# Optimization experiments

Measured on AMD Instinct MI355X. Metric: run time of the kernel, lower is better.

The kernel has to match this reference:

```python
import jax, jax.numpy as jnp
import numpy as np

D, Z, A, H, E = 1024, 256, 32, 512, 1024  # deterministic, state, action, stochastic(hidden), embedding
MIN_STD = 0.1


def _linear_params(key, out_dim, in_dim, scale=0.02):
    kw, kb = jax.random.split(key)
    W = jax.random.normal(kw, (out_dim, in_dim), jnp.float32) * scale
    b = jax.random.normal(kb, (out_dim,), jnp.float32) * scale
    return W, b


def setup_inputs() -> dict:
    key = jax.random.key(0)
    ks = jax.random.split(key, 16)
    T, B = 64, 512
    inp = {
        "prev_state": jax.random.normal(ks[0], (B, Z), jnp.float32),
        "prev_belief": jax.random.normal(ks[1], (B, D), jnp.float32),
        "actions": jax.random.normal(ks[2], (T, B, A), jnp.float32),
        "observations": jax.random.normal(ks[3], (T, B, E), jnp.float32),
        "nonterminals": jnp.ones((T, B, 1), jnp.float32),
        "noise_belief": jax.random.normal(ks[4], (T, B, D), jnp.float32),
        "noise_prior": jax.random.normal(ks[5], (T, B, Z), jnp.float32),
        "noise_post": jax.random.normal(ks[6], (T, B, Z), jnp.float32),
    }
    inp["W_sa"], inp["b_sa"] = _linear_params(ks[7], D, Z + A)      # fc_embed_state_action
    inp["W_ih"], inp["b_ih"] = _linear_params(ks[8], 3 * D, D)       # GRUCell input weights
    inp["W_hh"], inp["b_hh"] = _linear_params(ks[9], 3 * D, D)       # GRUCell hidden weights
    inp["W_eb"], inp["b_eb"] = _linear_params(ks[10], H, D)          # fc_embed_belief
    inp["W_bq"], inp["b_bq"] = _linear_params(ks[11], 2 * D, H)      # fc_belief_posterior
    inp["W_ebp"], inp["b_ebp"] = _linear_params(ks[12], H, D)        # fc_embed_belief_prior
    inp["W_sp"], inp["b_sp"] = _linear_params(ks[13], 2 * Z, H)      # fc_state_prior
    inp["W_ebq"], inp["b_ebq"] = _linear_params(ks[14], H, D + E)    # fc_embed_belief_posterior
    inp["W_sq"], inp["b_sq"] = _linear_params(ks[15], 2 * Z, H)      # fc_state_posterior
    return inp


def _gru_cell(x, h, W_ih, b_ih, W_hh, b_hh):
    gi = x @ W_ih.T + b_ih
    gh = h @ W_hh.T + b_hh
    i_r, i_z, i_n = jnp.split(gi, 3, axis=-1)
    h_r, h_z, h_n = jnp.split(gh, 3, axis=-1)
    r = jax.nn.sigmoid(i_r + h_r)
    z = jax.nn.sigmoid(i_z + h_z)
    n = jnp.tanh(i_n + r * h_n)
    return (1.0 - z) * n + z * h


def rssm_scan(prev_state, prev_belief, actions, observations, nonterminals,
              noise_belief, noise_prior, noise_post,
              W_sa, b_sa, W_ih, b_ih, W_hh, b_hh, W_eb, b_eb, W_bq, b_bq,
              W_ebp, b_ebp, W_sp, b_sp, W_ebq, b_ebq, W_sq, b_sq):
    # t==0 skips the nonterminal mask; shift nonterminals by one and prepend ones
    nt_seq = jnp.concatenate([jnp.ones_like(nonterminals[:1]), nonterminals[:-1]], axis=0)

    def step(carry, xs):
        belief, state = carry
        a_t, o_t, nt_t, nb_t, np_t, nq_t = xs
        s = state * nt_t
        deter_hidden = jax.nn.relu(jnp.concatenate([s, a_t], axis=1) @ W_sa.T + b_sa)
        rnn_out = _gru_cell(deter_hidden, belief, W_ih, b_ih, W_hh, b_hh)
        # stochastic belief
        sh = jax.nn.relu(rnn_out @ W_eb.T + b_eb)
        b_mean, b_raw_std = jnp.split(sh @ W_bq.T + b_bq, 2, axis=1)
        b_std = jax.nn.softplus(b_raw_std) + MIN_STD
        new_belief = b_mean + b_std * nb_t
        # prior
        sh_p = jax.nn.relu(new_belief @ W_ebp.T + b_ebp)
        p_mean, p_raw_std = jnp.split(sh_p @ W_sp.T + b_sp, 2, axis=1)
        p_std = jax.nn.softplus(p_raw_std) + MIN_STD
        p_state = p_mean + p_std * np_t
        # posterior (observations provided)
        sh_q = jax.nn.relu(jnp.concatenate([new_belief, o_t], axis=1) @ W_ebq.T + b_ebq)
        q_mean, q_raw_std = jnp.split(sh_q @ W_sq.T + b_sq, 2, axis=1)
        q_std = jax.nn.softplus(q_raw_std) + MIN_STD
        q_state = q_mean + q_std * nq_t
        return (new_belief, q_state), (new_belief, p_state, p_mean, p_std, q_state, q_mean, q_std)

    xs = (actions, observations, nt_seq, noise_belief, noise_prior, noise_post)
    _, ys = jax.lax.scan(step, (prev_belief, prev_state), xs)
    return ys  # each [T, B, dim]


def reference(prev_state, prev_belief, actions, observations, nonterminals,
              noise_belief, noise_prior, noise_post,
              W_sa, b_sa, W_ih, b_ih, W_hh, b_hh, W_eb, b_eb, W_bq, b_bq,
              W_ebp, b_ebp, W_sp, b_sp, W_ebq, b_ebq, W_sq, b_sq):
    return rssm_scan(prev_state, prev_belief, actions, observations, nonterminals,
                     noise_belief, noise_prior, noise_post,
                     W_sa, b_sa, W_ih, b_ih, W_hh, b_hh, W_eb, b_eb, W_bq, b_bq,
                     W_ebp, b_ebp, W_sp, b_sp, W_ebq, b_ebq, W_sq, b_sq)
```

## Files before the change

### kernel.cpp

```cpp
#include <hip/hip_runtime.h>
#include <hip/hip_bf16.h>
#include <math.h>


using bf16 = __hip_bfloat16;
using short8 = __attribute__((ext_vector_type(8))) short;
using f32x4 = __attribute__((ext_vector_type(4))) float;

__device__ __forceinline__ float sp_f(float x) { return x > 15.f ? x : log1pf(__expf(x)); }
__device__ __forceinline__ float sg_f(float x) { return 1.f / (1.f + __expf(-x)); }

struct GArgs {
  const bf16* Ab;
  const float* Af;
  const bf16* Bw;
  const float* bias;
  float* Cf;
  bf16* Cb;
  const float* addmat;
  const float* s_src;
  const float* nt_src;
  const float* act_src;
  int M, N, K, ldb, ldc, ldadd;
};

template<int ASRC, int EPI>
__device__ void gemm_core(const GArgs g, int bid) {
  __shared__ bf16 As[128 * 32];
  __shared__ bf16 Bs[128 * 32];
  const int ntiles = g.N >> 7;
  const int mt = bid / ntiles, nt = bid % ntiles;
  const int tid = threadIdx.x;
  const int l = tid & 63, w = tid >> 6;
  const int wm = w >> 1, wn = w & 1;
  const int l4r = l >> 2, l4b = l & 3;
  const int fl = l & 15, fg = l >> 4;
  f32x4 acc[4][4] = {};

  for (int k0 = 0; k0 < g.K; k0 += 32) {
    if constexpr (ASRC == 0) {
#pragma unroll
      for (int i = 0; i < 2; ++i) {
        const int r = w * 32 + i * 16;
        const bf16* gp = g.Ab + (size_t)(mt * 128 + r + l4r) * g.K + k0 + l4b * 8;
        __builtin_amdgcn_global_load_lds((const __attribute__((address_space(1))) void*)gp,
                                         (__attribute__((address_space(3))) void*)(As + r * 32),
                                         16, 0, 0);
      }
    } else {
#pragma unroll
      for (int p = 0; p < 2; ++p) {
        const int e = p * 2048 + tid * 8;
        const int r = e >> 5, c = e & 31;
        const int rg = mt * 128 + r;
        float4 x0, x1;
        if constexpr (ASRC == 1) {
          const float* src = g.Af + (size_t)rg * g.K + k0 + c;
          x0 = *(const float4*)src; x1 = *(const float4*)(src + 4);
        } else {
          const int kg = k0 + c;
          if (kg < 256) {
            const float* src = g.s_src + rg * 256 + kg;
            x0 = *(const float4*)src; x1 = *(const float4*)(src + 4);
            const float ntv = g.nt_src ? g.nt_src[rg] : 1.f;
            x0.x *= ntv; x0.y *= ntv; x0.z *= ntv; x0.w *= ntv;
            x1.x *= ntv; x1.y *= ntv; x1.z *= ntv; x1.w *= ntv;
          } else {
            const float* src = g.act_src + rg * 32 + (kg - 256);
            x0 = *(const float4*)src; x1 = *(const float4*)(src + 4);
          }
        }
        bf16 tb[8] __attribute__((aligned(16)));
        tb[0] = __float2bfloat16(x0.x); tb[1] = __float2bfloat16(x0.y);
        tb[2] = __float2bfloat16(x0.z); tb[3] = __float2bfloat16(x0.w);
        tb[4] = __float2bfloat16(x1.x); tb[5] = __float2bfloat16(x1.y);
        tb[6] = __float2bfloat16(x1.z); tb[7] = __float2bfloat16(x1.w);
        *(short8*)(As + e) = *(const short8*)tb;
      }
    }
#pragma unroll
    for (int i = 0; i < 2; ++i) {
      const int r = w * 32 + i * 16;
      const bf16* gp = g.Bw + (size_t)(nt * 128 + r + l4r) * g.ldb + k0 + l4b * 8;
      __builtin_amdgcn_global_load_lds((const __attribute__((address_space(1))) void*)gp,
                                       (__attribute__((address_space(3))) void*)(Bs + r * 32),
                                       16, 0, 0);
    }
    __syncthreads();
    short8 afr[4], bfr[4];
#pragma unroll
    for (int i = 0; i < 4; ++i)
      afr[i] = *(const short8*)(As + (wm * 64 + i * 16 + fl) * 32 + fg * 8);
#pragma unroll
    for (int i = 0; i < 4; ++i)
      bfr[i] = *(const short8*)(Bs + (wn * 64 + i * 16 + fl) * 32 + fg * 8);
#pragma unroll
    for (int mf = 0; mf < 4; ++mf)
#pragma unroll
      for (int nf = 0; nf < 4; ++nf)
        asm("v_mfma_f32_16x16x32_bf16 %0, %1, %2, %0"
            : "+v"(acc[mf][nf]) : "v"(afr[mf]), "v"(bfr[nf]));
    __syncthreads();
  }
#pragma unroll
  for (int mf = 0; mf < 4; ++mf) {
#pragma unroll
    for (int nf = 0; nf < 4; ++nf) {
      const int col = nt * 128 + wn * 64 + nf * 16 + fl;
      const float bv = g.bias ? g.bias[col] : 0.f;
#pragma unroll
      for (int r = 0; r < 4; ++r) {
        const int row = mt * 128 + wm * 64 + mf * 16 + fg * 4 + r;
        float v = acc[mf][nf][r] + bv;
        if constexpr (EPI == 2) v += g.addmat[(size_t)row * g.ldadd + col];
        if constexpr (EPI == 0) {
          g.Cf[(size_t)row * g.ldc + col] = v;
        } else {
          v = v > 0.f ? v : 0.f;
          g.Cb[(size_t)row * g.ldc + col] = __float2bfloat16(v);
        }
      }
    }
  }
}

template<int ASRC, int EPI>
__global__ __launch_bounds__(256) void gemm_k(GArgs g) { gemm_core<ASRC, EPI>(g, blockIdx.x); }

__global__ __launch_bounds__(256) void gemm2_k(GArgs g0, GArgs g1, int nb0) {
  if ((int)blockIdx.x < nb0) gemm_core<0, 0>(g0, blockIdx.x);
  else                       gemm_core<0, 0>(g1, blockIdx.x - nb0);
}

__global__ __launch_bounds__(256) void cvt_k(const float* __restrict__ src, bf16* __restrict__ dst, int n4) {
  int i = blockIdx.x * 256 + threadIdx.x;
  if (i >= n4) return;
  float4 v = ((const float4*)src)[i];
  bf16 t[4] __attribute__((aligned(8)));
  t[0] = __float2bfloat16(v.x); t[1] = __float2bfloat16(v.y);
  t[2] = __float2bfloat16(v.z); t[3] = __float2bfloat16(v.w);
  ((uint2*)dst)[i] = *(const uint2*)t;
}

__global__ __launch_bounds__(256) void gates_k(const float* __restrict__ gi, const float* __restrict__ gh,
                                               const bf16* __restrict__ hprev, bf16* __restrict__ rnn) {
  int i = blockIdx.x * 256 + threadIdx.x;
  if (i >= 512 * 1024) return;
  int m = i >> 10, n = i & 1023;
  const float* gim = gi + (size_t)m * 3072;
  const float* ghm = gh + (size_t)m * 3072;
  float r = sg_f(gim[n] + ghm[n]);
  float z = sg_f(gim[1024 + n] + ghm[1024 + n]);
  float nn = tanhf(gim[2048 + n] + r * ghm[2048 + n]);
  float h = __bfloat162float(hprev[i]);
  rnn[i] = __float2bfloat16((1.f - z) * nn + z * h);
}

__global__ __launch_bounds__(256) void belief_k(const float* __restrict__ raw, const float* __restrict__ nb,
                                                float* __restrict__ obel, bf16* __restrict__ bbf) {
  int i = blockIdx.x * 256 + threadIdx.x;
  if (i >= 512 * 1024) return;
  int m = i >> 10, n = i & 1023;
  float mean = raw[(size_t)m * 2048 + n];
  float rs = raw[(size_t)m * 2048 + 1024 + n];
  float sd = sp_f(rs) + 0.1f;
  float b = mean + sd * nb[i];
  obel[i] = b;
  bbf[i] = __float2bfloat16(b);
}

__global__ __launch_bounds__(256) void qpost_k(const float* __restrict__ raw, const float* __restrict__ noise,
                                               float* __restrict__ om, float* __restrict__ os,
                                               float* __restrict__ ost, int n) {
  int i = blockIdx.x * 256 + threadIdx.x;
  if (i >= n) return;
  int m = i >> 8, z = i & 255;
  float mean = raw[(size_t)m * 512 + z];
  float rs = raw[(size_t)m * 512 + 256 + z];
  float sd = sp_f(rs) + 0.1f;
  om[i] = mean; os[i] = sd; ost[i] = mean + sd * noise[i];
}

extern "C" void kernel_launch(void* const* d_in, const int* in_sizes, int n_in,
                              void* d_out, int out_size, void* d_ws, size_t ws_size,
                              hipStream_t stream) {
  const float* prev_state   = (const float*)d_in[0];
  const float* prev_belief  = (const float*)d_in[1];
  const float* actions      = (const float*)d_in[2];
  const float* observations = (const float*)d_in[3];
  const float* nonterm      = (const float*)d_in[4];
  const float* noise_belief = (const float*)d_in[5];
  const float* noise_prior  = (const float*)d_in[6];
  const float* noise_post   = (const float*)d_in[7];
  const float* W_sa  = (const float*)d_in[8];  const float* b_sa  = (const float*)d_in[9];
  const float* W_ih  = (const float*)d_in[10]; const float* b_ih  = (const float*)d_in[11];
  const float* W_hh  = (const float*)d_in[12]; const float* b_hh  = (const float*)d_in[13];
  const float* W_eb  = (const float*)d_in[14]; const float* b_eb  = (const float*)d_in[15];
  const float* W_bq  = (const float*)d_in[16]; const float* b_bq  = (const float*)d_in[17];
  const float* W_ebp = (const float*)d_in[18]; const float* b_ebp = (const float*)d_in[19];
  const float* W_sp  = (const float*)d_in[20]; const float* b_sp  = (const float*)d_in[21];
  const float* W_ebq = (const float*)d_in[22]; const float* b_ebq = (const float*)d_in[23];
  const float* W_sq  = (const float*)d_in[24]; const float* b_sq  = (const float*)d_in[25];

  float* out = (float*)d_out;
  const size_t off_bel = 0;
  const size_t off_pst = 33554432;
  const size_t off_pm  = 41943040;
  const size_t off_psd = 50331648;
  const size_t off_qst = 58720256;
  const size_t off_qm  = 67108864;
  const size_t off_qsd = 75497472;

  char* ws = (char*)d_ws;
  bf16* wbf   = (bf16*)ws;
  bf16* w_sa  = wbf;
  bf16* w_ih  = wbf + 294912;
  bf16* w_hh  = wbf + 3440640;
  bf16* w_eb  = wbf + 6586368;
  bf16* w_bq  = wbf + 7110656;
  bf16* w_ebp = wbf + 8159232;
  bf16* w_sp  = wbf + 8683520;
  bf16* w_ebq = wbf + 8945664;
  bf16* w_sq  = wbf + 9994240;
  size_t p = 20971520;
  bf16* bel_bf   = (bf16*)(ws + p); p += 1048576;
  bf16* deter_bf = (bf16*)(ws + p); p += 1048576;
  bf16* rnn_bf   = (bf16*)(ws + p); p += 1048576;
  bf16* sh_bf    = (bf16*)(ws + p); p += 524288;
  bf16* shq_bf   = (bf16*)(ws + p); p += 524288;
  float* p_raw = (float*)(ws + 25165824);
  float *gi, *gh, *bq_raw, *q_raw;
  if (ws_size >= 42991616ull) {
    gi     = (float*)(ws + 25165824);
    gh     = (float*)(ws + 31457280);
    bq_raw = (float*)(ws + 37748736);
    q_raw  = (float*)(ws + 41943040);
  } else {
    float* scratch = out + off_pst;
    gi = scratch; gh = scratch + 1572864; bq_raw = gh + 1572864; q_raw = bq_raw + 1048576;
  }

  auto cvt = [&](const float* s, bf16* d, int n) {
    int n4 = n >> 2;
    cvt_k<<<(n4 + 255) / 256, 256, 0, stream>>>(s, d, n4);
  };
  cvt(W_sa, w_sa, 294912);   cvt(W_ih, w_ih, 3145728);  cvt(W_hh, w_hh, 3145728);
  cvt(W_eb, w_eb, 524288);   cvt(W_bq, w_bq, 1048576);  cvt(W_ebp, w_ebp, 524288);
  cvt(W_sp, w_sp, 262144);   cvt(W_ebq, w_ebq, 1048576); cvt(W_sq, w_sq, 262144);
  cvt(prev_belief, bel_bf, 524288);

  float* obs_c = out + off_pm;
  {
    GArgs g{}; g.Af = observations; g.Bw = w_ebq + 1024; g.ldb = 2048; g.bias = b_ebq;
    g.Cf = obs_c; g.ldc = 512; g.M = 32768; g.N = 512; g.K = 1024;
    gemm_k<1, 0><<<1024, 256, 0, stream>>>(g);
  }

  for (int t = 0; t < 64; ++t) {
    {
      GArgs g{};
      g.s_src  = (t == 0) ? prev_state : out + off_qst + (size_t)(t - 1) * 131072;
      g.nt_src = (t == 0) ? nullptr : nonterm + (size_t)(t - 1) * 512;
      g.act_src = actions + (size_t)t * 16384;
      g.Bw = w_sa; g.ldb = 288; g.bias = b_sa; g.Cb = deter_bf; g.ldc = 1024;
      g.M = 512; g.N = 1024; g.K = 288;
      gemm_k<2, 1><<<32, 256, 0, stream>>>(g);
    }
    {
      GArgs g0{}; g0.Ab = deter_bf; g0.Bw = w_ih; g0.ldb = 1024; g0.bias = b_ih;
      g0.Cf = gi; g0.ldc = 3072; g0.M = 512; g0.N = 3072; g0.K = 1024;
      GArgs g1 = g0; g1.Ab = bel_bf; g1.Bw = w_hh; g1.bias = b_hh; g1.Cf = gh;
      gemm2_k<<<192, 256, 0, stream>>>(g0, g1, 96);
    }
    gates_k<<<2048, 256, 0, stream>>>(gi, gh, bel_bf, rnn_bf);
    {
      GArgs g{}; g.Ab = rnn_bf; g.Bw = w_eb; g.ldb = 1024; g.bias = b_eb;
      g.Cb = sh_bf; g.ldc = 512; g.M = 512; g.N = 512; g.K = 1024;
      gemm_k<0, 1><<<16, 256, 0, stream>>>(g);
    }
    {
      GArgs g{}; g.Ab = sh_bf; g.Bw = w_bq; g.ldb = 512; g.bias = b_bq;
      g.Cf = bq_raw; g.ldc = 2048; g.M = 512; g.N = 2048; g.K = 512;
      gemm_k<0, 0><<<64, 256, 0, stream>>>(g);
    }
    belief_k<<<2048, 256, 0, stream>>>(bq_raw, noise_belief + (size_t)t * 524288,
                                       out + off_bel + (size_t)t * 524288, bel_bf);
    {
      GArgs g{}; g.Ab = bel_bf; g.Bw = w_ebq; g.ldb = 2048;
      g.addmat = obs_c + (size_t)t * 262144; g.ldadd = 512;
      g.Cb = shq_bf; g.ldc = 512; g.M = 512; g.N = 512; g.K = 1024;
      gemm_k<0, 2><<<16, 256, 0, stream>>>(g);
    }
    {
      GArgs g{}; g.Ab = shq_bf; g.Bw = w_sq; g.ldb = 512; g.bias = b_sq;
      g.Cf = q_raw; g.ldc = 512; g.M = 512; g.N = 512; g.K = 512;
      gemm_k<0, 0><<<16, 256, 0, stream>>>(g);
    }
    qpost_k<<<512, 256, 0, stream>>>(q_raw, noise_post + (size_t)t * 131072,
                                     out + off_qm + (size_t)t * 131072,
                                     out + off_qsd + (size_t)t * 131072,
                                     out + off_qst + (size_t)t * 131072, 131072);
  }

  bf16* shp = (bf16*)(out + off_pst);
  {
    GArgs g{}; g.Af = out + off_bel; g.Bw = w_ebp; g.ldb = 1024; g.bias = b_ebp;
    g.Cb = shp; g.ldc = 512; g.M = 32768; g.N = 512; g.K = 1024;
    gemm_k<1, 1><<<1024, 256, 0, stream>>>(g);
  }
  for (int c = 0; c < 16; ++c) {
    {
      GArgs g{}; g.Ab = shp + (size_t)c * 1048576; g.Bw = w_sp; g.ldb = 512; g.bias = b_sp;
      g.Cf = p_raw; g.ldc = 512; g.M = 2048; g.N = 512; g.K = 512;
      gemm_k<0, 0><<<64, 256, 0, stream>>>(g);
    }
    qpost_k<<<2048, 256, 0, stream>>>(p_raw, noise_prior + (size_t)c * 524288,
                                      out + off_pm + (size_t)c * 524288,
                                      out + off_psd + (size_t)c * 524288,
                                      out + off_pst + (size_t)c * 524288, 524288);
  }
}
```

Measured before the change: 10.07 ms.

## Replace per-step kernel launches with persistent kernel using grid barriers and fused epilogues

Replaces the many per-timestep GEMM and elementwise launches with one persistent kernel of 128 blocks that synchronises stages through a hand-written global atomic barrier. The GRU input and hidden GEMMs are merged by interleaving reordered weights, so the gate math, belief sampling and posterior sampling run in GEMM epilogues instead of in separate kernels over fp32 scratch. LDS tiles grow to K=64 with an XOR swizzle and double-buffered async loads. This targets launch overhead and intermediate memory traffic in the sequential scan. It risks deadlock if all 128 blocks are not co-resident, and adds barrier latency at every stage.

```diff
diff --git a/kernel.cpp b/kernel.cpp
--- a/kernel.cpp
+++ b/kernel.cpp
@@ -7,178 +7,455 @@
 using short8 = __attribute__((ext_vector_type(8))) short;
 using f32x4 = __attribute__((ext_vector_type(4))) float;
 
-__device__ __forceinline__ float sp_f(float x) { return x > 15.f ? x : log1pf(__expf(x)); }
-__device__ __forceinline__ float sg_f(float x) { return 1.f / (1.f + __expf(-x)); }
-
-struct GArgs {
-  const bf16* Ab;
-  const float* Af;
-  const bf16* Bw;
-  const float* bias;
-  float* Cf;
-  bf16* Cb;
-  const float* addmat;
-  const float* s_src;
-  const float* nt_src;
-  const float* act_src;
-  int M, N, K, ldb, ldc, ldadd;
-};
-
-template<int ASRC, int EPI>
-__device__ void gemm_core(const GArgs g, int bid) {
-  __shared__ bf16 As[128 * 32];
-  __shared__ bf16 Bs[128 * 32];
-  const int ntiles = g.N >> 7;
-  const int mt = bid / ntiles, nt = bid % ntiles;
-  const int tid = threadIdx.x;
-  const int l = tid & 63, w = tid >> 6;
-  const int wm = w >> 1, wn = w & 1;
-  const int l4r = l >> 2, l4b = l & 3;
-  const int fl = l & 15, fg = l >> 4;
-  f32x4 acc[4][4] = {};
-
-  for (int k0 = 0; k0 < g.K; k0 += 32) {
-    if constexpr (ASRC == 0) {
-#pragma unroll
-      for (int i = 0; i < 2; ++i) {
-        const int r = w * 32 + i * 16;
-        const bf16* gp = g.Ab + (size_t)(mt * 128 + r + l4r) * g.K + k0 + l4b * 8;
-        __builtin_amdgcn_global_load_lds((const __attribute__((address_space(1))) void*)gp,
-                                         (__attribute__((address_space(3))) void*)(As + r * 32),
-                                         16, 0, 0);
-      }
-    } else {
-#pragma unroll
-      for (int p = 0; p < 2; ++p) {
-        const int e = p * 2048 + tid * 8;
-        const int r = e >> 5, c = e & 31;
-        const int rg = mt * 128 + r;
-        float4 x0, x1;
-        if constexpr (ASRC == 1) {
-          const float* src = g.Af + (size_t)rg * g.K + k0 + c;
-          x0 = *(const float4*)src; x1 = *(const float4*)(src + 4);
-        } else {
-          const int kg = k0 + c;
-          if (kg < 256) {
-            const float* src = g.s_src + rg * 256 + kg;
-            x0 = *(const float4*)src; x1 = *(const float4*)(src + 4);
-            const float ntv = g.nt_src ? g.nt_src[rg] : 1.f;
-            x0.x *= ntv; x0.y *= ntv; x0.z *= ntv; x0.w *= ntv;
-            x1.x *= ntv; x1.y *= ntv; x1.z *= ntv; x1.w *= ntv;
-          } else {
-            const float* src = g.act_src + rg * 32 + (kg - 256);
-            x0 = *(const float4*)src; x1 = *(const float4*)(src + 4);
-          }
-        }
-        bf16 tb[8] __attribute__((aligned(16)));
-        tb[0] = __float2bfloat16(x0.x); tb[1] = __float2bfloat16(x0.y);
-        tb[2] = __float2bfloat16(x0.z); tb[3] = __float2bfloat16(x0.w);
-        tb[4] = __float2bfloat16(x1.x); tb[5] = __float2bfloat16(x1.y);
-        tb[6] = __float2bfloat16(x1.z); tb[7] = __float2bfloat16(x1.w);
-        *(short8*)(As + e) = *(const short8*)tb;
-      }
-    }
-#pragma unroll
-    for (int i = 0; i < 2; ++i) {
-      const int r = w * 32 + i * 16;
-      const bf16* gp = g.Bw + (size_t)(nt * 128 + r + l4r) * g.ldb + k0 + l4b * 8;
-      __builtin_amdgcn_global_load_lds((const __attribute__((address_space(1))) void*)gp,
-                                       (__attribute__((address_space(3))) void*)(Bs + r * 32),
-                                       16, 0, 0);
+#define GRID 128
+
+__device__ __forceinline__ float sp_f(float x){ return x > 15.f ? x : log1pf(__expf(x)); }
+__device__ __forceinline__ float sg_f(float x){ return 1.f/(1.f+__expf(-x)); }
+__device__ __forceinline__ float b2f(bf16 x){ return __bfloat162float(x); }
+__device__ __forceinline__ bf16  f2b(float x){ return __float2bfloat16(x); }
+
+__device__ __forceinline__ int lds_off(int row, int slot){ return row*64 + (((slot ^ (row & 7))) << 3); }
+
+__device__ __forceinline__ void gbar(int* arrive, int* go, int ev) {
+  __threadfence();
+  __syncthreads();
+  if (blockIdx.x == 0) {
+    const int t = threadIdx.x;
+    if (t > 0 && t < GRID) {
+      while (__hip_atomic_load(&arrive[t], __ATOMIC_ACQUIRE, __HIP_MEMORY_SCOPE_AGENT) < ev)
+        __builtin_amdgcn_s_sleep(1);
     }
     __syncthreads();
-    short8 afr[4], bfr[4];
+    if (t == 0) __hip_atomic_store(go, ev, __ATOMIC_RELEASE, __HIP_MEMORY_SCOPE_AGENT);
+  } else {
+    if (threadIdx.x == 0) {
+      __hip_atomic_store(&arrive[blockIdx.x], ev, __ATOMIC_RELEASE, __HIP_MEMORY_SCOPE_AGENT);
+      while (__hip_atomic_load(go, __ATOMIC_ACQUIRE, __HIP_MEMORY_SCOPE_AGENT) < ev)
+        __builtin_amdgcn_s_sleep(1);
+    }
+  }
+  __syncthreads();
+  __threadfence();
+}
+
+__device__ __forceinline__ void glds_tile(const bf16* base, int ld, bf16* buf, int w, int l) {
+  const int rsub = l >> 3;
+  const int slot = (l & 7) ^ rsub;
+  const bf16* src = base + (size_t)(w*32 + rsub)*ld + slot*8;
+#pragma unroll
+  for (int i = 0; i < 4; ++i)
+    __builtin_amdgcn_global_load_lds((const __attribute__((address_space(1))) void*)(src + (size_t)(i*8)*ld),
+                                     (__attribute__((address_space(3))) void*)(buf + (w*32 + i*8)*64),
+                                     16, 0, 0);
+}
+
+__device__ __forceinline__ void mfma_tiles(f32x4 acc[4][4], const bf16* bA, const bf16* bB,
+                                           int wm, int wn, int fl, int fg) {
+#pragma unroll
+  for (int ks = 0; ks < 2; ++ks) {
+    short8 af[4], bfr[4];
 #pragma unroll
     for (int i = 0; i < 4; ++i)
-      afr[i] = *(const short8*)(As + (wm * 64 + i * 16 + fl) * 32 + fg * 8);
+      af[i] = *(const short8*)(bA + lds_off(wm*64 + i*16 + fl, ks*4 + fg));
 #pragma unroll
     for (int i = 0; i < 4; ++i)
-      bfr[i] = *(const short8*)(Bs + (wn * 64 + i * 16 + fl) * 32 + fg * 8);
+      bfr[i] = *(const short8*)(bB + lds_off(wn*64 + i*16 + fl, ks*4 + fg));
 #pragma unroll
     for (int mf = 0; mf < 4; ++mf)
 #pragma unroll
       for (int nf = 0; nf < 4; ++nf)
         asm("v_mfma_f32_16x16x32_bf16 %0, %1, %2, %0"
-            : "+v"(acc[mf][nf]) : "v"(afr[mf]), "v"(bfr[nf]));
-    __syncthreads();
-  }
-#pragma unroll
-  for (int mf = 0; mf < 4; ++mf) {
+            : "+v"(acc[mf][nf]) : "v"(af[mf]), "v"(bfr[nf]));
+  }
+}
+
+template<bool GRUA>
+__device__ __forceinline__ void kloop_async(const bf16* A0, const bf16* A1, int lda,
+    const bf16* Bw, int ldb, int K, int mt, int nt, f32x4 acc[4][4],
+    int w, int l, int wm, int wn, int fl, int fg,
+    bf16* sA0, bf16* sA1, bf16* sB0, bf16* sB1) {
+  bf16* bufA[2] = {sA0, sA1};
+  bf16* bufB[2] = {sB0, sB1};
+  const int nk = K >> 6;
+  glds_tile(A0 + (size_t)(mt*128)*lda, lda, bufA[0], w, l);
+  glds_tile(Bw + (size_t)(nt*128)*ldb, ldb, bufB[0], w, l);
+#pragma unroll 1
+  for (int ki = 0; ki < nk; ++ki) {
+    const int kn = ki + 1;
+    if (kn < nk) {
+      const int k0 = kn << 6;
+      const bf16* As; int kc;
+      if (GRUA && k0 >= 1024) { As = A1; kc = k0 - 1024; } else { As = A0; kc = k0; }
+      glds_tile(As + (size_t)(mt*128)*lda + kc, lda, bufA[kn & 1], w, l);
+      glds_tile(Bw + (size_t)(nt*128)*ldb + k0, ldb, bufB[kn & 1], w, l);
+      asm volatile("s_waitcnt vmcnt(8)" ::: "memory");
+    } else {
+      asm volatile("s_waitcnt vmcnt(0)" ::: "memory");
+    }
+    __builtin_amdgcn_s_barrier();
+    asm volatile("" ::: "memory");
+    mfma_tiles(acc, bufA[ki & 1], bufB[ki & 1], wm, wn, fl, fg);
+    asm volatile("" ::: "memory");
+    __builtin_amdgcn_s_barrier();
+    asm volatile("" ::: "memory");
+  }
+}
+
+__device__ __forceinline__ void kloop_sync_f32(const float* A, int lda, const bf16* Bw, int ldb,
+    int K, int mt, int nt, f32x4 acc[4][4],
+    int tid, int w, int l, int wm, int wn, int fl, int fg, bf16* sA0, bf16* sB0) {
+  const int nk = K >> 6;
+#pragma unroll 1
+  for (int ki = 0; ki < nk; ++ki) {
+    const int k0 = ki << 6;
+    glds_tile(Bw + (size_t)(nt*128)*ldb + k0, ldb, sB0, w, l);
+#pragma unroll
+    for (int i = 0; i < 4; ++i) {
+      const int sid = tid + (i << 8);
+      const int row = sid >> 3, s = sid & 7;
+      const float* src = A + (size_t)(mt*128 + row)*lda + k0 + s*8;
+      float4 a = ((const float4*)src)[0], b = ((const float4*)src)[1];
+      bf16 t8[8] __attribute__((aligned(16)));
+      t8[0]=f2b(a.x); t8[1]=f2b(a.y); t8[2]=f2b(a.z); t8[3]=f2b(a.w);
+      t8[4]=f2b(b.x); t8[5]=f2b(b.y); t8[6]=f2b(b.z); t8[7]=f2b(b.w);
+      *(short8*)(sA0 + lds_off(row, s)) = *(const short8*)t8;
+    }
+    asm volatile("s_waitcnt vmcnt(0) lgkmcnt(0)" ::: "memory");
+    __builtin_amdgcn_s_barrier();
+    asm volatile("" ::: "memory");
+    mfma_tiles(acc, sA0, sB0, wm, wn, fl, fg);
+    asm volatile("" ::: "memory");
+    __builtin_amdgcn_s_barrier();
+    asm volatile("" ::: "memory");
+  }
+}
+
+__device__ __forceinline__ void kloop_sa(const float* st, const float* ntp, const float* act,
+    const bf16* Bw, int mt, int nt, f32x4 acc[4][4],
+    int tid, int w, int l, int wm, int wn, int fl, int fg, bf16* sA0, bf16* sB0) {
+#pragma unroll 1
+  for (int ki = 0; ki < 5; ++ki) {
+    const int k0 = ki << 6;
+    glds_tile(Bw + (size_t)(nt*128)*320 + k0, 320, sB0, w, l);
+#pragma unroll
+    for (int i = 0; i < 4; ++i) {
+      const int sid = tid + (i << 8);
+      const int row = sid >> 3, s = sid & 7;
+      const int rg = mt*128 + row;
+      const int kg = k0 + s*8;
+      float4 a = {0,0,0,0}, b = {0,0,0,0};
+      if (kg < 256) {
+        const float* src = st + (size_t)rg*256 + kg;
+        a = ((const float4*)src)[0]; b = ((const float4*)src)[1];
+        const float nv = ntp ? ntp[rg] : 1.f;
+        a.x*=nv; a.y*=nv; a.z*=nv; a.w*=nv; b.x*=nv; b.y*=nv; b.z*=nv; b.w*=nv;
+      } else if (kg < 288) {
+        const float* src = act + (size_t)rg*32 + (kg - 256);
+        a = ((const float4*)src)[0]; b = ((const float4*)src)[1];
+      }
+      bf16 t8[8] __attribute__((aligned(16)));
+      t8[0]=f2b(a.x); t8[1]=f2b(a.y); t8[2]=f2b(a.z); t8[3]=f2b(a.w);
+      t8[4]=f2b(b.x); t8[5]=f2b(b.y); t8[6]=f2b(b.z); t8[7]=f2b(b.w);
+      *(short8*)(sA0 + lds_off(row, s)) = *(const short8*)t8;
+    }
+    asm volatile("s_waitcnt vmcnt(0) lgkmcnt(0)" ::: "memory");
+    __builtin_amdgcn_s_barrier();
+    asm volatile("" ::: "memory");
+    mfma_tiles(acc, sA0, sB0, wm, wn, fl, fg);
+    asm volatile("" ::: "memory");
+    __builtin_amdgcn_s_barrier();
+    asm volatile("" ::: "memory");
+  }
+}
+
+template<bool RELU, bool ADD>
+__device__ __forceinline__ void epi_bf16(const f32x4 acc[4][4], bf16* dst, int ldc,
+    const float* bias, const bf16* addm, int lda2, int mt, int nt, int wm, int wn, int fl, int fg) {
+#pragma unroll
+  for (int mf = 0; mf < 4; ++mf)
 #pragma unroll
     for (int nf = 0; nf < 4; ++nf) {
-      const int col = nt * 128 + wn * 64 + nf * 16 + fl;
-      const float bv = g.bias ? g.bias[col] : 0.f;
+      const int col = nt*128 + wn*64 + nf*16 + fl;
+      const float bv = bias ? bias[col] : 0.f;
 #pragma unroll
       for (int r = 0; r < 4; ++r) {
-        const int row = mt * 128 + wm * 64 + mf * 16 + fg * 4 + r;
+        const int row = mt*128 + wm*64 + mf*16 + fg*4 + r;
         float v = acc[mf][nf][r] + bv;
-        if constexpr (EPI == 2) v += g.addmat[(size_t)row * g.ldadd + col];
-        if constexpr (EPI == 0) {
-          g.Cf[(size_t)row * g.ldc + col] = v;
-        } else {
-          v = v > 0.f ? v : 0.f;
-          g.Cb[(size_t)row * g.ldc + col] = __float2bfloat16(v);
-        }
+        if (ADD) v += b2f(addm[(size_t)row*lda2 + col]);
+        if (RELU) v = v > 0.f ? v : 0.f;
+        dst[(size_t)row*ldc + col] = f2b(v);
       }
     }
-  }
-}
-
-template<int ASRC, int EPI>
-__global__ __launch_bounds__(256) void gemm_k(GArgs g) { gemm_core<ASRC, EPI>(g, blockIdx.x); }
-
-__global__ __launch_bounds__(256) void gemm2_k(GArgs g0, GArgs g1, int nb0) {
-  if ((int)blockIdx.x < nb0) gemm_core<0, 0>(g0, blockIdx.x);
-  else                       gemm_core<0, 0>(g1, blockIdx.x - nb0);
-}
-
-__global__ __launch_bounds__(256) void cvt_k(const float* __restrict__ src, bf16* __restrict__ dst, int n4) {
-  int i = blockIdx.x * 256 + threadIdx.x;
-  if (i >= n4) return;
-  float4 v = ((const float4*)src)[i];
-  bf16 t[4] __attribute__((aligned(8)));
-  t[0] = __float2bfloat16(v.x); t[1] = __float2bfloat16(v.y);
-  t[2] = __float2bfloat16(v.z); t[3] = __float2bfloat16(v.w);
-  ((uint2*)dst)[i] = *(const uint2*)t;
-}
-
-__global__ __launch_bounds__(256) void gates_k(const float* __restrict__ gi, const float* __restrict__ gh,
-                                               const bf16* __restrict__ hprev, bf16* __restrict__ rnn) {
-  int i = blockIdx.x * 256 + threadIdx.x;
-  if (i >= 512 * 1024) return;
-  int m = i >> 10, n = i & 1023;
-  const float* gim = gi + (size_t)m * 3072;
-  const float* ghm = gh + (size_t)m * 3072;
-  float r = sg_f(gim[n] + ghm[n]);
-  float z = sg_f(gim[1024 + n] + ghm[1024 + n]);
-  float nn = tanhf(gim[2048 + n] + r * ghm[2048 + n]);
-  float h = __bfloat162float(hprev[i]);
-  rnn[i] = __float2bfloat16((1.f - z) * nn + z * h);
-}
-
-__global__ __launch_bounds__(256) void belief_k(const float* __restrict__ raw, const float* __restrict__ nb,
-                                                float* __restrict__ obel, bf16* __restrict__ bbf) {
-  int i = blockIdx.x * 256 + threadIdx.x;
-  if (i >= 512 * 1024) return;
-  int m = i >> 10, n = i & 1023;
-  float mean = raw[(size_t)m * 2048 + n];
-  float rs = raw[(size_t)m * 2048 + 1024 + n];
-  float sd = sp_f(rs) + 0.1f;
-  float b = mean + sd * nb[i];
-  obel[i] = b;
-  bbf[i] = __float2bfloat16(b);
-}
-
-__global__ __launch_bounds__(256) void qpost_k(const float* __restrict__ raw, const float* __restrict__ noise,
-                                               float* __restrict__ om, float* __restrict__ os,
-                                               float* __restrict__ ost, int n) {
-  int i = blockIdx.x * 256 + threadIdx.x;
-  if (i >= n) return;
-  int m = i >> 8, z = i & 255;
-  float mean = raw[(size_t)m * 512 + z];
-  float rs = raw[(size_t)m * 512 + 256 + z];
-  float sd = sp_f(rs) + 0.1f;
-  om[i] = mean; os[i] = sd; ost[i] = mean + sd * noise[i];
+}
+
+__device__ __forceinline__ void epi_gru(const f32x4 acc[4][4], const float* bg,
+    const bf16* bel, bf16* rnn, int mt, int nt, int wm, int wn, int fl, int fg) {
+  const int cb = nt*128 + wn*64;
+  const int j = nt*32 + wn*16 + fl;
+  const float b0 = bg[cb + fl], b1 = bg[cb + 16 + fl], b2 = bg[cb + 32 + fl], b3 = bg[cb + 48 + fl];
+#pragma unroll
+  for (int mf = 0; mf < 4; ++mf)
+#pragma unroll
+    for (int r = 0; r < 4; ++r) {
+      const int row = mt*128 + wm*64 + mf*16 + fg*4 + r;
+      const float a0 = acc[mf][0][r] + b0;
+      const float a1 = acc[mf][1][r] + b1;
+      const float a2 = acc[mf][2][r] + b2;
+      const float a3 = acc[mf][3][r] + b3;
+      const float rr = sg_f(a0), zz = sg_f(a1);
+      const float nn = tanhf(a2 + rr*a3);
+      const float h = b2f(bel[(size_t)row*1024 + j]);
+      rnn[(size_t)row*1024 + j] = f2b((1.f - zz)*nn + zz*h);
+    }
+}
+
+__device__ __forceinline__ void epi_bq(const f32x4 acc[4][4], const float* bb,
+    const float* nb, float* obel, bf16* belbf, int mt, int nt, int wm, int wn, int fl, int fg) {
+  const int cb = nt*128 + wn*64;
+#pragma unroll
+  for (int g = 0; g < 2; ++g) {
+    const int j = nt*64 + (wn*2 + g)*16 + fl;
+    const float bm = bb[cb + g*32 + fl];
+    const float bs = bb[cb + g*32 + 16 + fl];
+#pragma unroll
+    for (int mf = 0; mf < 4; ++mf)
+#pragma unroll
+      for (int r = 0; r < 4; ++r) {
+        const int row = mt*128 + wm*64 + mf*16 + fg*4 + r;
+        const float mean = acc[mf][2*g][r] + bm;
+        const float sd = sp_f(acc[mf][2*g+1][r] + bs) + 0.1f;
+        const float bl = mean + sd * nb[(size_t)row*1024 + j];
+        obel[(size_t)row*1024 + j] = bl;
+        belbf[(size_t)row*1024 + j] = f2b(bl);
+      }
+  }
+}
+
+__device__ __forceinline__ void epi_qp(const f32x4 acc[4][4], const float* bb, const float* noise,
+    float* om, float* os, float* ost, int mt, int nt, int wm, int wn, int fl, int fg) {
+  const int cb = nt*128 + wn*64;
+#pragma unroll
+  for (int g = 0; g < 2; ++g) {
+    const int j = nt*64 + (wn*2 + g)*16 + fl;
+    const float bm = bb[cb + g*32 + fl];
+    const float bs = bb[cb + g*32 + 16 + fl];
+#pragma unroll
+    for (int mf = 0; mf < 4; ++mf)
+#pragma unroll
+      for (int r = 0; r < 4; ++r) {
+        const int row = mt*128 + wm*64 + mf*16 + fg*4 + r;
+        const float mean = acc[mf][2*g][r] + bm;
+        const float sd = sp_f(acc[mf][2*g+1][r] + bs) + 0.1f;
+        const size_t o = (size_t)row*256 + j;
+        om[o] = mean; os[o] = sd; ost[o] = mean + sd*noise[o];
+      }
+  }
+}
+
+struct PP {
+  const float *prev_state, *prev_belief, *actions, *obs, *nonterm, *nb, *np, *nq;
+  const float *b_sa, *b_eb, *b_ebq, *b_ebp;
+  const bf16 *w_sa, *w_gru, *w_eb, *w_bq, *w_ebq, *w_sq, *w_ebp, *w_sp;
+  const float *bg, *bbq, *bsq, *bsp;
+  bf16 *obs_c, *deter, *bel, *rnn, *sh, *shq, *shp;
+  float *o_bel, *o_pst, *o_pm, *o_psd, *o_qst, *o_qm, *o_qsd;
+  int *arrive; int *go;
+};
+
+__global__ __launch_bounds__(256) void persist_k(PP p) {
+  __shared__ bf16 sA[2][8192];
+  __shared__ bf16 sB[2][8192];
+  const int bid = blockIdx.x, tid = threadIdx.x;
+  const int l = tid & 63, w = tid >> 6;
+  const int wm = w >> 1, wn = w & 1, fl = l & 15, fg = l >> 4;
+  int ev = 1;
+
+#pragma unroll 1
+  for (int i = bid*256 + tid; i < 65536; i += GRID*256) {
+    float4 a = ((const float4*)p.prev_belief)[i*2];
+    float4 b = ((const float4*)p.prev_belief)[i*2 + 1];
+    bf16 t8[8] __attribute__((aligned(16)));
+    t8[0]=f2b(a.x); t8[1]=f2b(a.y); t8[2]=f2b(a.z); t8[3]=f2b(a.w);
+    t8[4]=f2b(b.x); t8[5]=f2b(b.y); t8[6]=f2b(b.z); t8[7]=f2b(b.w);
+    ((short8*)p.bel)[i] = *(const short8*)t8;
+  }
+#pragma unroll 1
+  for (int tt = bid; tt < 1024; tt += GRID) {
+    const int mt = tt >> 2, nt = tt & 3;
+    f32x4 acc[4][4] = {};
+    kloop_sync_f32(p.obs, 1024, p.w_ebq + 1024, 2048, 1024, mt, nt, acc,
+                   tid, w, l, wm, wn, fl, fg, sA[0], sB[0]);
+    epi_bf16<false,false>(acc, p.obs_c, 512, p.b_ebq, nullptr, 0, mt, nt, wm, wn, fl, fg);
+  }
+  gbar(p.arrive, p.go, ev++);
+
+#pragma unroll 1
+  for (int t = 0; t < 64; ++t) {
+    if (bid < 32) {
+      const int mt = bid >> 3, nt = bid & 7;
+      f32x4 acc[4][4] = {};
+      const float* ss  = t ? (p.o_qst + (size_t)(t-1)*131072) : p.prev_state;
+      const float* ntp = t ? (p.nonterm + (size_t)(t-1)*512) : nullptr;
+      kloop_sa(ss, ntp, p.actions + (size_t)t*16384, p.w_sa, mt, nt, acc,
+               tid, w, l, wm, wn, fl, fg, sA[0], sB[0]);
+      epi_bf16<true,false>(acc, p.deter, 1024, p.b_sa, nullptr, 0, mt, nt, wm, wn, fl, fg);
+    }
+    gbar(p.arrive, p.go, ev++);
+    {
+      const int mt = bid >> 5, nt = bid & 31;
+      f32x4 acc[4][4] = {};
+      kloop_async<true>(p.deter, p.bel, 1024, p.w_gru, 2048, 2048, mt, nt, acc,
+                        w, l, wm, wn, fl, fg, sA[0], sA[1], sB[0], sB[1]);
+      epi_gru(acc, p.bg, p.bel, p.rnn, mt, nt, wm, wn, fl, fg);
+    }
+    gbar(p.arrive, p.go, ev++);
+    if (bid < 16) {
+      const int mt = bid >> 2, nt = bid & 3;
+      f32x4 acc[4][4] = {};
+      kloop_async<false>(p.rnn, nullptr, 1024, p.w_eb, 1024, 1024, mt, nt, acc,
+                         w, l, wm, wn, fl, fg, sA[0], sA[1], sB[0], sB[1]);
+      epi_bf16<true,false>(acc, p.sh, 512, p.b_eb, nullptr, 0, mt, nt, wm, wn, fl, fg);
+    }
+    gbar(p.arrive, p.go, ev++);
+    if (bid < 64) {
+      const int mt = bid >> 4, nt = bid & 15;
+      f32x4 acc[4][4] = {};
+      kloop_async<false>(p.sh, nullptr, 512, p.w_bq, 512, 512, mt, nt, acc,
+                         w, l, wm, wn, fl, fg, sA[0], sA[1], sB[0], sB[1]);
+      epi_bq(acc, p.bbq, p.nb + (size_t)t*524288, p.o_bel + (size_t)t*524288, p.bel,
+             mt, nt, wm, wn, fl, fg);
+    }
+    gbar(p.arrive, p.go, ev++);
+    if (bid < 16) {
+      const int mt = bid >> 2, nt = bid & 3;
+      f32x4 acc[4][4] = {};
+      kloop_async<false>(p.bel, nullptr, 1024, p.w_ebq, 2048, 1024, mt, nt, acc,
+                         w, l, wm, wn, fl, fg, sA[0], sA[1], sB[0], sB[1]);
+      epi_bf16<true,true>(acc, p.shq, 512, nullptr, p.obs_c + (size_t)t*262144, 512,
+                          mt, nt, wm, wn, fl, fg);
+    }
+    gbar(p.arrive, p.go, ev++);
+    if (bid < 16) {
+      const int mt = bid >> 2, nt = bid & 3;
+      f32x4 acc[4][4] = {};
+      kloop_async<false>(p.shq, nullptr, 512, p.w_sq, 512, 512, mt, nt, acc,
+                         w, l, wm, wn, fl, fg, sA[0], sA[1], sB[0], sB[1]);
+      epi_qp(acc, p.bsq, p.nq + (size_t)t*131072,
+             p.o_qm + (size_t)t*131072, p.o_qsd + (size_t)t*131072, p.o_qst + (size_t)t*131072,
+             mt, nt, wm, wn, fl, fg);
+    }
+    gbar(p.arrive, p.go, ev++);
+  }
+
+#pragma unroll 1
+  for (int tt = bid; tt < 1024; tt += GRID) {
+    const int mt = tt >> 2, nt = tt & 3;
+    f32x4 acc[4][4] = {};
+    kloop_sync_f32(p.o_bel, 1024, p.w_ebp, 1024, 1024, mt, nt, acc,
+                   tid, w, l, wm, wn, fl, fg, sA[0], sB[0]);
+    epi_bf16<true,false>(acc, p.shp, 512, p.b_ebp, nullptr, 0, mt, nt, wm, wn, fl, fg);
+  }
+  gbar(p.arrive, p.go, ev++);
+#pragma unroll 1
+  for (int c = 0; c < 8; ++c) {
+    const int mt = c*32 + (bid >> 2), nt = bid & 3;
+    f32x4 acc[4][4] = {};
+    kloop_async<false>(p.shp, nullptr, 512, p.w_sp, 512, 512, mt, nt, acc,
+                       w, l, wm, wn, fl, fg, sA[0], sA[1], sB[0], sB[1]);
+    gbar(p.arrive, p.go, ev++);
+    epi_qp(acc, p.bsp, p.np, p.o_pm, p.o_psd, p.o_pst, mt, nt, wm, wn, fl, fg);
+  }
+}
+
+__global__ __launch_bounds__(256) void k_cvt8(const float* __restrict__ s, bf16* __restrict__ d, int n8) {
+  int i = blockIdx.x*256 + threadIdx.x;
+  if (i >= n8) return;
+  float4 a = ((const float4*)s)[i*2], b = ((const float4*)s)[i*2+1];
+  bf16 t8[8] __attribute__((aligned(16)));
+  t8[0]=f2b(a.x); t8[1]=f2b(a.y); t8[2]=f2b(a.z); t8[3]=f2b(a.w);
+  t8[4]=f2b(b.x); t8[5]=f2b(b.y); t8[6]=f2b(b.z); t8[7]=f2b(b.w);
+  ((short8*)d)[i] = *(const short8*)t8;
+}
+
+__global__ __launch_bounds__(256) void k_wsa(const float* __restrict__ W, bf16* __restrict__ dst) {
+  int i = blockIdx.x*256 + threadIdx.x;
+  if (i >= 40960) return;
+  int e = i*8, r = e/320, c = e - r*320;
+  bf16 t8[8] __attribute__((aligned(16)));
+  if (c < 288) {
+    const float* s = W + (size_t)r*288 + c;
+    float4 a = ((const float4*)s)[0], b = ((const float4*)s)[1];
+    t8[0]=f2b(a.x); t8[1]=f2b(a.y); t8[2]=f2b(a.z); t8[3]=f2b(a.w);
+    t8[4]=f2b(b.x); t8[5]=f2b(b.y); t8[6]=f2b(b.z); t8[7]=f2b(b.w);
+  } else {
+    for (int q = 0; q < 8; ++q) t8[q] = f2b(0.f);
+  }
+  *(short8*)(dst + e) = *(const short8*)t8;
+}
+
+__global__ __launch_bounds__(256) void k_gru_r(const float* __restrict__ Wih, const float* __restrict__ Whh,
+                                               bf16* __restrict__ dst) {
+  int idx = blockIdx.x*256 + threadIdx.x;
+  if (idx >= 2097152) return;
+  int rp = idx >> 9;
+  int c4 = (idx & 511) << 2;
+  int nt = rp >> 7, id = rp & 127;
+  int wn2 = (id >> 6) & 1, nf = (id >> 4) & 3, fl2 = id & 15;
+  int j = nt*32 + wn2*16 + fl2;
+  float4 v = {0,0,0,0};
+  if (c4 < 1024) {
+    int srow = (nf==0) ? j : (nf==1) ? 1024+j : (nf==2) ? 2048+j : -1;
+    if (srow >= 0) v = *(const float4*)(Wih + (size_t)srow*1024 + c4);
+  } else {
+    int srow = (nf==0) ? j : (nf==1) ? 1024+j : (nf==3) ? 2048+j : -1;
+    if (srow >= 0) v = *(const float4*)(Whh + (size_t)srow*1024 + (c4-1024));
+  }
+  bf16 t4[4] __attribute__((aligned(8)));
+  t4[0]=f2b(v.x); t4[1]=f2b(v.y); t4[2]=f2b(v.z); t4[3]=f2b(v.w);
+  *(uint2*)(dst + (size_t)rp*2048 + c4) = *(const uint2*)t4;
+}
+
+__global__ __launch_bounds__(256) void k_pair(const float* __restrict__ src, bf16* __restrict__ dst,
+                                              int halfN, int n) {
+  int idx = blockIdx.x*256 + threadIdx.x;
+  if (idx >= n) return;
+  int rp = idx >> 7;
+  int c4 = (idx & 127) << 2;
+  int nt = rp >> 7, id = rp & 127;
+  int pb = (id >> 5) & 3, comp = (id >> 4) & 1, fl2 = id & 15;
+  int j = nt*64 + pb*16 + fl2;
+  int srow = comp*halfN + j;
+  float4 v = *(const float4*)(src + (size_t)srow*512 + c4);
+  bf16 t4[4] __attribute__((aligned(8)));
+  t4[0]=f2b(v.x); t4[1]=f2b(v.y); t4[2]=f2b(v.z); t4[3]=f2b(v.w);
+  *(uint2*)(dst + (size_t)rp*512 + c4) = *(const uint2*)t4;
+}
+
+__global__ __launch_bounds__(256) void k_bias(const float* b_ih, const float* b_hh, const float* b_bq,
+                                              const float* b_sq, const float* b_sp,
+                                              float* bg, float* bbq, float* bsq, float* bsp) {
+  for (int i = threadIdx.x; i < 4096; i += 256) {
+    int nt = i >> 7, id = i & 127;
+    int wn2 = (id >> 6) & 1, nf = (id >> 4) & 3, fl2 = id & 15;
+    int j = nt*32 + wn2*16 + fl2;
+    float v;
+    if (nf == 0) v = b_ih[j] + b_hh[j];
+    else if (nf == 1) v = b_ih[1024+j] + b_hh[1024+j];
+    else if (nf == 2) v = b_ih[2048+j];
+    else v = b_hh[2048+j];
+    bg[i] = v;
+  }
+  for (int i = threadIdx.x; i < 2048; i += 256) {
+    int nt = i >> 7, id = i & 127, pb = (id >> 5) & 3, comp = (id >> 4) & 1, fl2 = id & 15;
+    int j = nt*64 + pb*16 + fl2;
+    bbq[i] = b_bq[comp*1024 + j];
+  }
+  for (int i = threadIdx.x; i < 512; i += 256) {
+    int nt = i >> 7, id = i & 127, pb = (id >> 5) & 3, comp = (id >> 4) & 1, fl2 = id & 15;
+    int j = nt*64 + pb*16 + fl2;
+    bsq[i] = b_sq[comp*256 + j];
+    bsp[i] = b_sp[comp*256 + j];
+  }
 }
 
 extern "C" void kernel_launch(void* const* d_in, const int* in_sizes, int n_in,
@@ -203,120 +480,61 @@
   const float* W_sq  = (const float*)d_in[24]; const float* b_sq  = (const float*)d_in[25];
 
   float* out = (float*)d_out;
-  const size_t off_bel = 0;
-  const size_t off_pst = 33554432;
-  const size_t off_pm  = 41943040;
-  const size_t off_psd = 50331648;
-  const size_t off_qst = 58720256;
-  const size_t off_qm  = 67108864;
-  const size_t off_qsd = 75497472;
-
   char* ws = (char*)d_ws;
-  bf16* wbf   = (bf16*)ws;
-  bf16* w_sa  = wbf;
-  bf16* w_ih  = wbf + 294912;
-  bf16* w_hh  = wbf + 3440640;
-  bf16* w_eb  = wbf + 6586368;
-  bf16* w_bq  = wbf + 7110656;
-  bf16* w_ebp = wbf + 8159232;
-  bf16* w_sp  = wbf + 8683520;
-  bf16* w_ebq = wbf + 8945664;
-  bf16* w_sq  = wbf + 9994240;
-  size_t p = 20971520;
-  bf16* bel_bf   = (bf16*)(ws + p); p += 1048576;
-  bf16* deter_bf = (bf16*)(ws + p); p += 1048576;
-  bf16* rnn_bf   = (bf16*)(ws + p); p += 1048576;
-  bf16* sh_bf    = (bf16*)(ws + p); p += 524288;
-  bf16* shq_bf   = (bf16*)(ws + p); p += 524288;
-  float* p_raw = (float*)(ws + 25165824);
-  float *gi, *gh, *bq_raw, *q_raw;
-  if (ws_size >= 42991616ull) {
-    gi     = (float*)(ws + 25165824);
-    gh     = (float*)(ws + 31457280);
-    bq_raw = (float*)(ws + 37748736);
-    q_raw  = (float*)(ws + 41943040);
-  } else {
-    float* scratch = out + off_pst;
-    gi = scratch; gh = scratch + 1572864; bq_raw = gh + 1572864; q_raw = bq_raw + 1048576;
-  }
-
-  auto cvt = [&](const float* s, bf16* d, int n) {
-    int n4 = n >> 2;
-    cvt_k<<<(n4 + 255) / 256, 256, 0, stream>>>(s, d, n4);
-  };
-  cvt(W_sa, w_sa, 294912);   cvt(W_ih, w_ih, 3145728);  cvt(W_hh, w_hh, 3145728);
-  cvt(W_eb, w_eb, 524288);   cvt(W_bq, w_bq, 1048576);  cvt(W_ebp, w_ebp, 524288);
-  cvt(W_sp, w_sp, 262144);   cvt(W_ebq, w_ebq, 1048576); cvt(W_sq, w_sq, 262144);
-  cvt(prev_belief, bel_bf, 524288);
-
-  float* obs_c = out + off_pm;
-  {
-    GArgs g{}; g.Af = observations; g.Bw = w_ebq + 1024; g.ldb = 2048; g.bias = b_ebq;
-    g.Cf = obs_c; g.ldc = 512; g.M = 32768; g.N = 512; g.K = 1024;
-    gemm_k<1, 0><<<1024, 256, 0, stream>>>(g);
-  }
-
-  for (int t = 0; t < 64; ++t) {
-    {
-      GArgs g{};
-      g.s_src  = (t == 0) ? prev_state : out + off_qst + (size_t)(t - 1) * 131072;
-      g.nt_src = (t == 0) ? nullptr : nonterm + (size_t)(t - 1) * 512;
-      g.act_src = actions + (size_t)t * 16384;
-      g.Bw = w_sa; g.ldb = 288; g.bias = b_sa; g.Cb = deter_bf; g.ldc = 1024;
-      g.M = 512; g.N = 1024; g.K = 288;
-      gemm_k<2, 1><<<32, 256, 0, stream>>>(g);
-    }
-    {
-      GArgs g0{}; g0.Ab = deter_bf; g0.Bw = w_ih; g0.ldb = 1024; g0.bias = b_ih;
-      g0.Cf = gi; g0.ldc = 3072; g0.M = 512; g0.N = 3072; g0.K = 1024;
-      GArgs g1 = g0; g1.Ab = bel_bf; g1.Bw = w_hh; g1.bias = b_hh; g1.Cf = gh;
-      gemm2_k<<<192, 256, 0, stream>>>(g0, g1, 96);
-    }
-    gates_k<<<2048, 256, 0, stream>>>(gi, gh, bel_bf, rnn_bf);
-    {
-      GArgs g{}; g.Ab = rnn_bf; g.Bw = w_eb; g.ldb = 1024; g.bias = b_eb;
-      g.Cb = sh_bf; g.ldc = 512; g.M = 512; g.N = 512; g.K = 1024;
-      gemm_k<0, 1><<<16, 256, 0, stream>>>(g);
-    }
-    {
-      GArgs g{}; g.Ab = sh_bf; g.Bw = w_bq; g.ldb = 512; g.bias = b_bq;
-      g.Cf = bq_raw; g.ldc = 2048; g.M = 512; g.N = 2048; g.K = 512;
-      gemm_k<0, 0><<<64, 256, 0, stream>>>(g);
-    }
-    belief_k<<<2048, 256, 0, stream>>>(bq_raw, noise_belief + (size_t)t * 524288,
-                                       out + off_bel + (size_t)t * 524288, bel_bf);
-    {
-      GArgs g{}; g.Ab = bel_bf; g.Bw = w_ebq; g.ldb = 2048;
-      g.addmat = obs_c + (size_t)t * 262144; g.ldadd = 512;
-      g.Cb = shq_bf; g.ldc = 512; g.M = 512; g.N = 512; g.K = 1024;
-      gemm_k<0, 2><<<16, 256, 0, stream>>>(g);
-    }
-    {
-      GArgs g{}; g.Ab = shq_bf; g.Bw = w_sq; g.ldb = 512; g.bias = b_sq;
-      g.Cf = q_raw; g.ldc = 512; g.M = 512; g.N = 512; g.K = 512;
-      gemm_k<0, 0><<<16, 256, 0, stream>>>(g);
-    }
-    qpost_k<<<512, 256, 0, stream>>>(q_raw, noise_post + (size_t)t * 131072,
-                                     out + off_qm + (size_t)t * 131072,
-                                     out + off_qsd + (size_t)t * 131072,
-                                     out + off_qst + (size_t)t * 131072, 131072);
-  }
-
-  bf16* shp = (bf16*)(out + off_pst);
-  {
-    GArgs g{}; g.Af = out + off_bel; g.Bw = w_ebp; g.ldb = 1024; g.bias = b_ebp;
-    g.Cb = shp; g.ldc = 512; g.M = 32768; g.N = 512; g.K = 1024;
-    gemm_k<1, 1><<<1024, 256, 0, stream>>>(g);
-  }
-  for (int c = 0; c < 16; ++c) {
-    {
-      GArgs g{}; g.Ab = shp + (size_t)c * 1048576; g.Bw = w_sp; g.ldb = 512; g.bias = b_sp;
-      g.Cf = p_raw; g.ldc = 512; g.M = 2048; g.N = 512; g.K = 512;
-      gemm_k<0, 0><<<64, 256, 0, stream>>>(g);
-    }
-    qpost_k<<<2048, 256, 0, stream>>>(p_raw, noise_prior + (size_t)c * 524288,
-                                      out + off_pm + (size_t)c * 524288,
-                                      out + off_psd + (size_t)c * 524288,
-                                      out + off_pst + (size_t)c * 524288, 524288);
-  }
-}
+
+  int* arrive = (int*)ws;
+  int* go     = (int*)(ws + 512);
+  float* bg   = (float*)(ws + 1024);
+  float* bbq  = bg + 4096;
+  float* bsq  = bbq + 2048;
+  float* bsp  = bsq + 512;
+  bf16* wb    = (bf16*)(ws + 32768);
+  bf16* w_sa  = wb;
+  bf16* w_gru = wb + 327680;
+  bf16* w_eb  = wb + 8716288;
+  bf16* w_bq  = wb + 9240576;
+  bf16* w_ebq = wb + 10289152;
+  bf16* w_sq  = wb + 11337728;
+  bf16* w_ebp = wb + 11599872;
+  bf16* w_sp  = wb + 12124160;
+
+  float* o_bel = out;
+  float* o_pst = out + 33554432;
+  float* o_pm  = out + 41943040;
+  float* o_psd = out + 50331648;
+  float* o_qst = out + 58720256;
+  float* o_qm  = out + 67108864;
+  float* o_qsd = out + 75497472;
+  bf16* obs_c = (bf16*)o_pm;
+  bf16* shp   = (bf16*)o_pst;
+  bf16* deter = (bf16*)o_psd;
+  bf16* belb  = deter + 524288;
+  bf16* rnn   = belb + 524288;
+  bf16* sh    = rnn + 524288;
+  bf16* shq   = sh + 262144;
+
+  hipMemsetAsync(ws, 0, 1024, stream);
+  k_wsa  <<<160, 256, 0, stream>>>(W_sa, w_sa);
+  k_gru_r<<<8192, 256, 0, stream>>>(W_ih, W_hh, w_gru);
+  k_cvt8 <<<256, 256, 0, stream>>>(W_eb, w_eb, 65536);
+  k_pair <<<1024, 256, 0, stream>>>(W_bq, w_bq, 1024, 262144);
+  k_cvt8 <<<512, 256, 0, stream>>>(W_ebq, w_ebq, 131072);
+  k_pair <<<256, 256, 0, stream>>>(W_sq, w_sq, 256, 65536);
+  k_cvt8 <<<256, 256, 0, stream>>>(W_ebp, w_ebp, 65536);
+  k_pair <<<256, 256, 0, stream>>>(W_sp, w_sp, 256, 65536);
+  k_bias <<<1, 256, 0, stream>>>(b_ih, b_hh, b_bq, b_sq, b_sp, bg, bbq, bsq, bsp);
+
+  PP p;
+  p.prev_state = prev_state; p.prev_belief = prev_belief; p.actions = actions;
+  p.obs = observations; p.nonterm = nonterm; p.nb = noise_belief; p.np = noise_prior; p.nq = noise_post;
+  p.b_sa = b_sa; p.b_eb = b_eb; p.b_ebq = b_ebq; p.b_ebp = b_ebp;
+  p.w_sa = w_sa; p.w_gru = w_gru; p.w_eb = w_eb; p.w_bq = w_bq;
+  p.w_ebq = w_ebq; p.w_sq = w_sq; p.w_ebp = w_ebp; p.w_sp = w_sp;
+  p.bg = bg; p.bbq = bbq; p.bsq = bsq; p.bsp = bsp;
+  p.obs_c = obs_c; p.deter = deter; p.bel = belb; p.rnn = rnn; p.sh = sh; p.shq = shq; p.shp = shp;
+  p.o_bel = o_bel; p.o_pst = o_pst; p.o_pm = o_pm; p.o_psd = o_psd;
+  p.o_qst = o_qst; p.o_qm = o_qm; p.o_qsd = o_qsd;
+  p.arrive = arrive; p.go = go;
+
+  persist_k<<<GRID, 256, 0, stream>>>(p);
+}
```

Measured after the change: 29.64 ms. +194.3%, slower.
